# Performance work log

Hardware: AMD Instinct MI355X
Metric: run time of the kernel (lower is better)

## Reference

```python
import jax, jax.numpy as jnp
import numpy as np

BIN_ALPHA = 1.0  # alpha mixture factor from init
NEG_SLOPE = 0.1  # LeakyReLU slope


def setup_inputs() -> dict:
    key = jax.random.key(0)
    ks = jax.random.split(key, 10)
    B, N, BIN, D = 8, 19264, 100, 768
    gene_expression = jax.random.uniform(ks[0], (B, N), dtype=jnp.float32) * 10.0
    pad_mask = jax.random.randint(ks[1], (B, N), 0, 2, dtype=jnp.int32)
    masked_mask = jax.random.randint(ks[2], (B, N), 0, 2, dtype=jnp.int32)
    # layer1: Linear(1, BIN) -> weight (BIN,1) stored as (BIN,), bias (BIN,)
    w1 = jax.random.normal(ks[3], (BIN,), dtype=jnp.float32) * (1.0)
    b1 = jax.random.normal(ks[4], (BIN,), dtype=jnp.float32) * 0.1
    # layer2: Linear(BIN, BIN) -> weight (BIN,BIN), bias (BIN,)
    w2 = jax.random.normal(ks[5], (BIN, BIN), dtype=jnp.float32) * (1.0 / np.sqrt(BIN))
    b2 = jax.random.normal(ks[6], (BIN,), dtype=jnp.float32) * 0.1
    emb_table = jax.random.normal(ks[7], (BIN, D), dtype=jnp.float32)
    pad_emb = jax.random.normal(ks[8], (D,), dtype=jnp.float32)
    mask_emb = jax.random.normal(ks[9], (D,), dtype=jnp.float32)
    return {
        "gene_expression": gene_expression,
        "pad_mask": pad_mask,
        "masked_mask": masked_mask,
        "w1": w1, "b1": b1, "w2": w2, "b2": b2,
        "emb_table": emb_table, "pad_emb": pad_emb, "mask_emb": mask_emb,
    }


def reference(gene_expression, pad_mask, masked_mask, w1, b1, w2, b2,
              emb_table, pad_emb, mask_emb):
    # v1 = Linear(1, BIN): x[..., None] * w1 + b1 -> (B, N, BIN)
    v1 = gene_expression[..., None] * w1 + b1
    # LeakyReLU(0.1)
    v2 = jnp.where(v1 > 0, v1, NEG_SLOPE * v1)
    # cross-layer projection: v3 = alpha * v2 + Linear(BIN, BIN)(v2)
    v3 = BIN_ALPHA * v2 + jnp.einsum("bnk,jk->bnj", v2, w2) + b2
    weights = jax.nn.softmax(v3, axis=-1)          # (B, N, BIN)
    embeddings = jnp.einsum("bnk,kd->bnd", weights, emb_table)  # (B, N, D)
    # mixed_precision=True: pad/mask token embeddings are cast to bfloat16
    # before being scattered into the float32 output (then upcast on assign).
    pad_e = pad_emb.astype(jnp.bfloat16).astype(embeddings.dtype)
    mask_e = mask_emb.astype(jnp.bfloat16).astype(embeddings.dtype)
    embeddings = jnp.where((pad_mask != 0)[..., None], pad_e, embeddings)
    embeddings = jnp.where((masked_mask != 0)[..., None], mask_e, embeddings)
    return embeddings
```

## Files before the change

kernel.cpp:

```cpp
#include <hip/hip_runtime.h>
#include <hip/hip_bf16.h>

#define BINS 100
#define DIM 768
#define TPB 64
#define NTHREADS 256
#define KPAD 128
#define PITCH 136

#define OFF_ET    0
#define OFF_P     196608
#define OFF_Q     197120
#define OFF_RARE  197632
#define OFF_R     199680
#define OFF_W2PT  199744

typedef __attribute__((ext_vector_type(8))) short bf16x8;
typedef __attribute__((ext_vector_type(4))) float f32x4;
typedef __attribute__((ext_vector_type(16))) float f32x16;

__device__ __forceinline__ unsigned short f2bf(float x) {
    __hip_bfloat16 h = __float2bfloat16(x);
    return *reinterpret_cast<unsigned short*>(&h);
}
__device__ __forceinline__ float bfrt(float x) {
    return __bfloat162float(__float2bfloat16(x));
}
__device__ __forceinline__ f32x4 bfrt4(f32x4 v) {
    f32x4 r;
    r.x = bfrt(v.x); r.y = bfrt(v.y); r.z = bfrt(v.z); r.w = bfrt(v.w);
    return r;
}

__global__ void prep(const float* __restrict__ emb,
                     const float* __restrict__ w1,
                     const float* __restrict__ b1,
                     const float* __restrict__ w2,
                     const float* __restrict__ b2,
                     unsigned char* __restrict__ ws)
{
    const int bid = blockIdx.x;
    const int tid = threadIdx.x;
    if (bid < DIM) {
        unsigned short* et = (unsigned short*)(ws + OFF_ET);
        float v = (tid < BINS) ? emb[(long)tid * DIM + bid] : 0.f;
        et[bid * KPAD + tid] = f2bf(v);
        return;
    }
    const int j = bid - DIM;
    float* Pv   = (float*)(ws + OFF_P);
    float* Qv   = (float*)(ws + OFF_Q);
    f32x4* rare = (f32x4*)(ws + OFF_RARE);
    int*   Rp   = (int*)  (ws + OFF_R);
    float* w2pT = (float*)(ws + OFF_W2PT);

    __shared__ float pl[128], ql[128], tl[128];
    __shared__ float redP[128], redQ[128];

    if (tid < BINS) {
        float w = w1[tid], b = b1[tid];
        float f = (w > 0.f || (w == 0.f && b > 0.f)) ? 1.f : 0.1f;
        pl[tid] = w * f;
        ql[tid] = b * f;
        tl[tid] = (w != 0.f) ? (-b / w) : -1.f;
    } else {
        pl[tid] = 0.f; ql[tid] = 0.f; tl[tid] = -1.f;
    }
    __syncthreads();

    float pP = 0.f, pQ = 0.f;
    if (tid < BINS) {
        float w = w2[j * BINS + tid];
        pP = w * pl[tid];
        pQ = w * ql[tid];
        w2pT[tid * BINS + j] = w + (j == tid ? 1.f : 0.f);
    }
    redP[tid] = pP; redQ[tid] = pQ;
    __syncthreads();
    #pragma unroll
    for (int sft = 64; sft > 0; sft >>= 1) {
        if (tid < sft) { redP[tid] += redP[tid + sft]; redQ[tid] += redQ[tid + sft]; }
        __syncthreads();
    }
    if (tid == 0) {
        Pv[j] = pl[j] + redP[0];
        Qv[j] = ql[j] + b2[j] + redQ[0];
    }

    const float tj = tl[j];
    float pr = 0.f;
    if (tid < BINS) {
        float t2 = tl[tid];
        pr = (t2 > tj || (t2 == tj && tid < j)) ? 1.f : 0.f;
    }
    __syncthreads();
    redP[tid] = pr;
    __syncthreads();
    #pragma unroll
    for (int sft = 64; sft > 0; sft >>= 1) {
        if (tid < sft) redP[tid] += redP[tid + sft];
        __syncthreads();
    }
    if (tid == 0) {
        int rank = (int)redP[0];
        f32x4 e;
        e.x = tj; e.y = w1[j]; e.z = b1[j];
        e.w = __int_as_float(j);
        rare[rank] = e;
    }

    if (j == 0) {
        float pp = (tid < BINS && tl[tid] > 0.f) ? 1.f : 0.f;
        __syncthreads();
        redQ[tid] = pp;
        __syncthreads();
        #pragma unroll
        for (int sft = 64; sft > 0; sft >>= 1) {
            if (tid < sft) redQ[tid] += redQ[tid + sft];
            __syncthreads();
        }
        if (tid == 0) {
            *Rp = (int)redQ[0];
            f32x4 s; s.x = -1e30f; s.y = 0.f; s.z = 0.f; s.w = __int_as_float(0);
            rare[BINS] = s;
        }
    }
}

__global__ __launch_bounds__(NTHREADS, 8)
void ead_kernel(const float* __restrict__ gene,
                const int*   __restrict__ pad_mask,
                const int*   __restrict__ masked_mask,
                const unsigned short* __restrict__ et,
                const float* __restrict__ Pv,
                const float* __restrict__ Qv,
                const f32x4* __restrict__ rare,
                const int*   __restrict__ Rp,
                const float* __restrict__ w2pT,
                const float* __restrict__ pad_emb,
                const float* __restrict__ mask_emb,
                float* __restrict__ out,
                int T)
{
    __shared__ unsigned short wbf[TPB][PITCH];
    __shared__ float xs[TPB];
    __shared__ short surv[TPB];
    __shared__ short olist[TPB];
    __shared__ int Ssh, Osh;

    const int tid  = threadIdx.x;
    const int lane = tid & 63;
    const int wave = tid >> 6;

    const int nblk = (int)gridDim.x;
    const int bid  = (int)blockIdx.x;
    const int wg   = ((nblk & 7) == 0) ? ((bid & 7) * (nblk >> 3) + (bid >> 3))
                                       : bid;
    const long t0  = (long)wg * TPB;
    const int nvalid = min(TPB, (int)(T - t0));

    if (wave == 0) {
        int o = 3;
        if (lane < nvalid) {
            int pm  = pad_mask[t0 + lane];
            int msk = masked_mask[t0 + lane];
            o = msk ? 2 : (pm ? 1 : 0);
            xs[lane] = gene[t0 + lane];
        }
        unsigned long long bs = __ballot(o == 0);
        unsigned long long bo = __ballot(o == 1 || o == 2);
        int si = __popcll(bs & ((1ull << lane) - 1ull));
        int oi = __popcll(bo & ((1ull << lane) - 1ull));
        if (o == 0) surv[si] = (short)lane;
        if (o == 1 || o == 2) olist[oi] = (short)(lane | ((o == 2) ? 256 : 0));
        if (lane == 0) { Ssh = __popcll(bs); Osh = __popcll(bo); }
    }
    __syncthreads();
    const int S = Ssh, O = Osh;

    {
        const f32x4* pe = (const f32x4*)pad_emb;
        const f32x4* me = (const f32x4*)mask_emb;
        f32x4 p0 = bfrt4(pe[lane]), p1 = bfrt4(pe[lane + 64]), p2 = bfrt4(pe[lane + 128]);
        f32x4 m0 = bfrt4(me[lane]), m1 = bfrt4(me[lane + 64]), m2 = bfrt4(me[lane + 128]);
        for (int i = wave; i < O; i += 4) {
            int e = olist[i];
            int row = e & 63;
            bool mm = (e & 256) != 0;
            f32x4* orow = (f32x4*)(out + (t0 + row) * (long)DIM);
            __builtin_nontemporal_store(mm ? m0 : p0, orow + lane);
            __builtin_nontemporal_store(mm ? m1 : p1, orow + lane + 64);
            __builtin_nontemporal_store(mm ? m2 : p2, orow + lane + 128);
        }
    }

    {
        int s = wave + 4 * (lane >> 2);
        int part = lane & 3;
        const int j0 = part * 25;
        if (s < S) {
            float x = xs[surv[s]];
            float v3[25];
            #pragma unroll
            for (int i = 0; i < 25; i++)
                v3[i] = fmaf(x, Pv[j0 + i], Qv[j0 + i]);
            const int R = *Rp;
            for (int idx = 0; idx < R; ++idx) {
                f32x4 rr = rare[idx];
                if (rr.x <= x) break;
                float v1 = fmaf(x, rr.y, rr.z);
                float d = 0.9f * fabsf(v1);
                int k = __float_as_int(rr.w);
                const float* wc = w2pT + k * BINS + j0;
                #pragma unroll
                for (int i = 0; i < 25; i++)
                    v3[i] = fmaf(wc[i], d, v3[i]);
            }
            float vmax = -1e30f;
            #pragma unroll
            for (int i = 0; i < 25; i++) vmax = fmaxf(vmax, v3[i]);
            vmax = fmaxf(vmax, __shfl_xor(vmax, 1));
            vmax = fmaxf(vmax, __shfl_xor(vmax, 2));
            float sum = 0.f;
            #pragma unroll
            for (int i = 0; i < 25; i++) {
                v3[i] = __expf(v3[i] - vmax);
                sum += v3[i];
            }
            sum += __shfl_xor(sum, 1);
            sum += __shfl_xor(sum, 2);
            float inv = 1.f / sum;
            #pragma unroll
            for (int i = 0; i < 25; i++)
                wbf[s][j0 + i] = f2bf(v3[i] * inv);
            if (part == 3) {
                #pragma unroll
                for (int j = BINS; j < KPAD; j += 2)
                    *reinterpret_cast<unsigned int*>(&wbf[s][j]) = 0u;
            }
        }
    }
    __syncthreads();

    if (S > 0) {
        const int col  = lane & 31;
        const int half = lane >> 5;
        const int nmt = (S > 32) ? 2 : 1;
        for (int mtile = 0; mtile < nmt; mtile++) {
            const unsigned short* arow = &wbf[mtile * 32 + col][half * 8];
            bf16x8 a0 = *(const bf16x8*)(arow);
            bf16x8 a1 = *(const bf16x8*)(arow + 16);
            bf16x8 a2 = *(const bf16x8*)(arow + 32);
            bf16x8 a3 = *(const bf16x8*)(arow + 48);
            bf16x8 a4 = *(const bf16x8*)(arow + 64);
            bf16x8 a5 = *(const bf16x8*)(arow + 80);
            bf16x8 a6 = *(const bf16x8*)(arow + 96);
            bf16x8 a7 = *(const bf16x8*)(arow + 112);
            for (int ct = 0; ct < 6; ct++) {
                int cbase = (wave * 6 + ct) * 32;
                const unsigned short* bp = et + (long)(cbase + col) * KPAD + half * 8;
                f32x16 acc;
                #pragma unroll
                for (int r = 0; r < 16; r++) acc[r] = 0.f;
                acc = __builtin_amdgcn_mfma_f32_32x32x16_bf16(a0, *(const bf16x8*)(bp),       acc, 0, 0, 0);
                acc = __builtin_amdgcn_mfma_f32_32x32x16_bf16(a1, *(const bf16x8*)(bp + 16),  acc, 0, 0, 0);
                acc = __builtin_amdgcn_mfma_f32_32x32x16_bf16(a2, *(const bf16x8*)(bp + 32),  acc, 0, 0, 0);
                acc = __builtin_amdgcn_mfma_f32_32x32x16_bf16(a3, *(const bf16x8*)(bp + 48),  acc, 0, 0, 0);
                acc = __builtin_amdgcn_mfma_f32_32x32x16_bf16(a4, *(const bf16x8*)(bp + 64),  acc, 0, 0, 0);
                acc = __builtin_amdgcn_mfma_f32_32x32x16_bf16(a5, *(const bf16x8*)(bp + 80),  acc, 0, 0, 0);
                acc = __builtin_amdgcn_mfma_f32_32x32x16_bf16(a6, *(const bf16x8*)(bp + 96),  acc, 0, 0, 0);
                acc = __builtin_amdgcn_mfma_f32_32x32x16_bf16(a7, *(const bf16x8*)(bp + 112), acc, 0, 0, 0);
                #pragma unroll
                for (int r = 0; r < 16; r++) {
                    int row = (r & 3) + 8 * (r >> 2) + 4 * half + mtile * 32;
                    if (row < S) {
                        int tkn = surv[row];
                        __builtin_nontemporal_store(
                            acc[r], out + (t0 + tkn) * (long)DIM + cbase + col);
                    }
                }
            }
        }
    }
}

extern "C" void kernel_launch(void* const* d_in, const int* in_sizes, int n_in,
                              void* d_out, int out_size, void* d_ws, size_t ws_size,
                              hipStream_t stream) {
    const float* gene  = (const float*)d_in[0];
    const int*   pm    = (const int*)  d_in[1];
    const int*   mm    = (const int*)  d_in[2];
    const float* w1    = (const float*)d_in[3];
    const float* b1    = (const float*)d_in[4];
    const float* w2    = (const float*)d_in[5];
    const float* b2    = (const float*)d_in[6];
    const float* emb   = (const float*)d_in[7];
    const float* pade  = (const float*)d_in[8];
    const float* maske = (const float*)d_in[9];
    float* out = (float*)d_out;
    unsigned char* ws = (unsigned char*)d_ws;

    int T = in_sizes[0];
    int nblk = (T + TPB - 1) / TPB;

    hipLaunchKernelGGL(prep, dim3(DIM + BINS), dim3(128), 0, stream,
                       emb, w1, b1, w2, b2, ws);
    hipLaunchKernelGGL(ead_kernel, dim3(nblk), dim3(NTHREADS), 0, stream,
                       gene, pm, mm,
                       (const unsigned short*)(ws + OFF_ET),
                       (const float*)(ws + OFF_P),
                       (const float*)(ws + OFF_Q),
                       (const f32x4*)(ws + OFF_RARE),
                       (const int*)(ws + OFF_R),
                       (const float*)(ws + OFF_W2PT),
                       pade, maske, out, T);
}
```

Baseline: 138.7 us.

## Split pad/mask row writes into dedicated blocks separate from softmax-GEMM blocks

The single kernel now launches two kinds of blocks. The first nov blocks each handle 256 rows and only write pad/mask embeddings, using a wave-wide shuffle loop over that wave's 64 rows. The remaining blocks compute softmax and MFMA only for surviving rows, and exit early when a tile has none. The aim is to take the store-only work off the compute blocks so they spend less time per block. The cost is extra mask reads, a serial per-row loop in the overwrite blocks, and possible load imbalance between the two block types.

After: 152.7 us. 10.0% more time.

```diff
diff --git a/kernel.cpp b/kernel.cpp
--- a/kernel.cpp
+++ b/kernel.cpp
@@ -7,6 +7,7 @@
 #define NTHREADS 256
 #define KPAD 128
 #define PITCH 136
+#define ROWS_OV 256
 
 #define OFF_ET    0
 #define OFF_P     196608
@@ -140,59 +141,64 @@
                 const float* __restrict__ pad_emb,
                 const float* __restrict__ mask_emb,
                 float* __restrict__ out,
-                int T)
+                int nov, int T)
 {
-    __shared__ unsigned short wbf[TPB][PITCH];
-    __shared__ float xs[TPB];
-    __shared__ short surv[TPB];
-    __shared__ short olist[TPB];
-    __shared__ int Ssh, Osh;
-
     const int tid  = threadIdx.x;
     const int lane = tid & 63;
     const int wave = tid >> 6;
 
-    const int nblk = (int)gridDim.x;
-    const int bid  = (int)blockIdx.x;
-    const int wg   = ((nblk & 7) == 0) ? ((bid & 7) * (nblk >> 3) + (bid >> 3))
-                                       : bid;
-    const long t0  = (long)wg * TPB;
-    const int nvalid = min(TPB, (int)(T - t0));
-
-    if (wave == 0) {
-        int o = 3;
-        if (lane < nvalid) {
-            int pm  = pad_mask[t0 + lane];
-            int msk = masked_mask[t0 + lane];
-            o = msk ? 2 : (pm ? 1 : 0);
-            xs[lane] = gene[t0 + lane];
-        }
-        unsigned long long bs = __ballot(o == 0);
-        unsigned long long bo = __ballot(o == 1 || o == 2);
-        int si = __popcll(bs & ((1ull << lane) - 1ull));
-        int oi = __popcll(bo & ((1ull << lane) - 1ull));
-        if (o == 0) surv[si] = (short)lane;
-        if (o == 1 || o == 2) olist[oi] = (short)(lane | ((o == 2) ? 256 : 0));
-        if (lane == 0) { Ssh = __popcll(bs); Osh = __popcll(bo); }
-    }
-    __syncthreads();
-    const int S = Ssh, O = Osh;
-
-    {
+    if ((int)blockIdx.x < nov) {
+        const long r0 = (long)blockIdx.x * ROWS_OV + wave * 64;
+        int pmv = 0, mmv = 0;
+        if (r0 + lane < T) {
+            pmv = pad_mask[r0 + lane];
+            mmv = masked_mask[r0 + lane];
+        }
         const f32x4* pe = (const f32x4*)pad_emb;
         const f32x4* me = (const f32x4*)mask_emb;
         f32x4 p0 = bfrt4(pe[lane]), p1 = bfrt4(pe[lane + 64]), p2 = bfrt4(pe[lane + 128]);
         f32x4 m0 = bfrt4(me[lane]), m1 = bfrt4(me[lane + 64]), m2 = bfrt4(me[lane + 128]);
-        for (int i = wave; i < O; i += 4) {
-            int e = olist[i];
-            int row = e & 63;
-            bool mm = (e & 256) != 0;
-            f32x4* orow = (f32x4*)(out + (t0 + row) * (long)DIM);
-            __builtin_nontemporal_store(mm ? m0 : p0, orow + lane);
-            __builtin_nontemporal_store(mm ? m1 : p1, orow + lane + 64);
-            __builtin_nontemporal_store(mm ? m2 : p2, orow + lane + 128);
-        }
-    }
+        const int nrow = (int)(min((long)T, r0 + 64) - r0);
+        for (int i = 0; i < nrow; i++) {
+            int pm = __shfl(pmv, i);
+            int mm = __shfl(mmv, i);
+            if (mm | pm) {
+                f32x4* orow = (f32x4*)(out + (r0 + i) * (long)DIM);
+                __builtin_nontemporal_store(mm ? m0 : p0, orow + lane);
+                __builtin_nontemporal_store(mm ? m1 : p1, orow + lane + 64);
+                __builtin_nontemporal_store(mm ? m2 : p2, orow + lane + 128);
+            }
+        }
+        return;
+    }
+
+    __shared__ unsigned short wbf[TPB][PITCH];
+    __shared__ float xs[TPB];
+    __shared__ short surv[TPB];
+    __shared__ int Ssh;
+
+    const int nsv = (int)gridDim.x - nov;
+    const int sb  = (int)blockIdx.x - nov;
+    const int wg  = ((nsv & 7) == 0) ? ((sb & 7) * (nsv >> 3) + (sb >> 3)) : sb;
+    const long t0 = (long)wg * TPB;
+    const int nvalid = min(TPB, (int)(T - t0));
+
+    if (wave == 0) {
+        int o = 1;
+        if (lane < nvalid) {
+            int pm  = pad_mask[t0 + lane];
+            int msk = masked_mask[t0 + lane];
+            o = (msk || pm) ? 1 : 0;
+            xs[lane] = gene[t0 + lane];
+        }
+        unsigned long long bs = __ballot(o == 0);
+        int si = __popcll(bs & ((1ull << lane) - 1ull));
+        if (o == 0) surv[si] = (short)lane;
+        if (lane == 0) Ssh = __popcll(bs);
+    }
+    __syncthreads();
+    const int S = Ssh;
+    if (S == 0) return;
 
     {
         int s = wave + 4 * (lane >> 2);
@@ -242,7 +248,7 @@
     }
     __syncthreads();
 
-    if (S > 0) {
+    {
         const int col  = lane & 31;
         const int half = lane >> 5;
         const int nmt = (S > 32) ? 2 : 1;
@@ -301,11 +307,12 @@
     unsigned char* ws = (unsigned char*)d_ws;
 
     int T = in_sizes[0];
-    int nblk = (T + TPB - 1) / TPB;
+    int nov = (T + ROWS_OV - 1) / ROWS_OV;
+    int nsv = (T + TPB - 1) / TPB;
 
     hipLaunchKernelGGL(prep, dim3(DIM + BINS), dim3(128), 0, stream,
                        emb, w1, b1, w2, b2, ws);
-    hipLaunchKernelGGL(ead_kernel, dim3(nblk), dim3(NTHREADS), 0, stream,
+    hipLaunchKernelGGL(ead_kernel, dim3(nov + nsv), dim3(NTHREADS), 0, stream,
                        gene, pm, mm,
                        (const unsigned short*)(ws + OFF_ET),
                        (const float*)(ws + OFF_P),
@@ -313,5 +320,5 @@
                        (const f32x4*)(ws + OFF_RARE),
                        (const int*)(ws + OFF_R),
                        (const float*)(ws + OFF_W2PT),
-                       pade, maske, out, T);
-}
+                       pade, maske, out, nov, T);
+}
```
